# Kernel optimization log

Hardware: AMD Instinct MI355X
Metric: run time of the kernel (lower is better)

The kernel has to match this reference:

```python
import math
import jax, jax.numpy as jnp
import numpy as np

PATCH = 32
NUM_ANG = 8
NUM_SP = 4
CLIPVAL = 0.2
EPS = 1e-10
BATCH = 16384


def _gaussian1d(ksize, sigma):
    x = jnp.arange(ksize, dtype=jnp.float32) - ksize // 2
    if ksize % 2 == 0:
        x = x + 0.5
    g = jnp.exp(-(x * x) / (2.0 * sigma * sigma))
    return g / jnp.sum(g)


def _sift_params(patch_size, num_spatial_bins):
    ksize = 2 * int(patch_size / (num_spatial_bins + 1))
    stride = patch_size // num_spatial_bins
    pad = ksize // 4
    return ksize, stride, pad


def setup_inputs() -> dict:
    key = jax.random.key(0)
    inp = jax.random.uniform(key, (BATCH, 1, PATCH, PATCH), dtype=jnp.float32)
    return {"input": inp}


def reference(input):
    B = input.shape[0]
    ps, n_ang, n_sp = PATCH, NUM_ANG, NUM_SP
    ksize, stride, pad = _sift_params(ps, n_sp)

    # Gaussian weighting kernel over the patch (sum-normalized), sigma = ps/sqrt(2)
    sigma = float(ps) / math.sqrt(2.0)
    g1 = _gaussian1d(ps, sigma)
    gk = jnp.outer(g1, g1)  # (ps, ps)

    # Triangular SIFT pooling kernel (ksize, ksize)
    ks_2 = float(ksize) / 2.0
    xc2 = ks_2 - jnp.abs(jnp.arange(ksize, dtype=jnp.float32) + 0.5 - ks_2)
    pk = jnp.outer(xc2, xc2) / (ks_2 ** 2)

    # spatial_gradient(mode='diff', normalized=True): replicate-pad, [-0.5,0,0.5]
    xp = jnp.pad(input, ((0, 0), (0, 0), (1, 1), (1, 1)), mode='edge')
    gx = 0.5 * (xp[:, :, 1:-1, 2:] - xp[:, :, 1:-1, :-2])
    gy = 0.5 * (xp[:, :, 2:, 1:-1] - xp[:, :, :-2, 1:-1])

    mag = jnp.sqrt(gx * gx + gy * gy + EPS) * gk  # gaussian-weighted magnitude
    ori = jnp.arctan2(gy, gx + EPS) + 2.0 * jnp.pi

    # soft binning into angular bins
    o_big = float(n_ang) * ori / (2.0 * jnp.pi)
    bo0f = jnp.floor(o_big)
    wo1_ = o_big - bo0f
    bo0 = jnp.mod(bo0f, n_ang).astype(jnp.int32)  # (B,1,ps,ps)
    bo1 = jnp.mod(bo0 + 1, n_ang)
    wo0 = (1.0 - wo1_) * mag
    wo1 = wo1_ * mag

    ib = jnp.arange(n_ang, dtype=jnp.int32).reshape(1, n_ang, 1, 1)
    # (B, n_ang, ps, ps): soft-assigned magnitude per angular bin
    ang = (bo0 == ib) * wo0 + (bo1 == ib) * wo1

    # per-bin spatial pooling conv (same kernel for every bin -> fold bins into batch)
    ang = ang.reshape(B * n_ang, 1, ps, ps)
    pooled = jax.lax.conv_general_dilated(
        ang, pk[None, None], (stride, stride), [(pad, pad), (pad, pad)],
        dimension_numbers=('NCHW', 'OIHW', 'NCHW'))  # (B*n_ang,1,n_sp,n_sp)
    desc = pooled.reshape(B, n_ang * n_sp * n_sp)

    def l2norm(x):
        return x / jnp.maximum(jnp.linalg.norm(x, axis=1, keepdims=True), 1e-12)

    desc = l2norm(desc)
    desc = jnp.clip(desc, 0.0, CLIPVAL)
    desc = l2norm(desc)
    # RootSIFT: sqrt of L1-normalized descriptor
    desc = jnp.sqrt(desc / jnp.maximum(jnp.sum(jnp.abs(desc), axis=1, keepdims=True), 1e-12) + EPS)
    return desc
```

## Files before the change

### kernel.cpp

```cpp
#include <hip/hip_runtime.h>
#include <hip/hip_fp16.h>
#include <math.h>

typedef __attribute__((ext_vector_type(8))) _Float16 f16x8;
typedef __attribute__((ext_vector_type(4))) float f32x4;
typedef __attribute__((ext_vector_type(2))) float f32x2;

static constexpr unsigned short f2h(float f) {
    if (f == 0.0f) return 0;
    unsigned u = __builtin_bit_cast(unsigned, f);
    int e = (int)((u >> 23) & 0xff) - 127 + 15;
    unsigned m = (u >> 13) & 0x3ff;
    return (unsigned short)((e << 10) | m);
}

struct alignas(16) WxTbl { unsigned short v[16 * 32]; };
static constexpr WxTbl gen_wx() {
    WxTbl t{};
    for (int n = 0; n < 16; ++n)
        for (int k = 0; k < 32; ++k) {
            float w = 0.0f;
            if (n < 4) {
                int kk = k - 8 * n + 3;
                if (kk >= 0 && kk < 12) {
                    float d = (float)kk - 5.5f; if (d < 0) d = -d;
                    w = 6.0f - d;
                }
            }
            t.v[n * 32 + k] = f2h(w);
        }
    return t;
}
__device__ const WxTbl WXT = gen_wx();

struct alignas(16) GTbl { float v[32]; };
static constexpr GTbl gen_g() {
    GTbl t{};
    for (int i = 0; i < 32; ++i) {
        double x = -((i - 15.5) * (i - 15.5)) / 1024.0;
        double s = 1.0, term = 1.0;
        for (int k = 1; k < 16; ++k) { term *= x / k; s += term; }
        t.v[i] = (float)s;
    }
    return t;
}
__device__ const GTbl GT = gen_g();

__global__ __launch_bounds__(256, 8) void sift_desc_kernel(
        const float* __restrict__ in, float* __restrict__ out) {
    __shared__ __align__(16) unsigned short ang[8192];

    const int b = blockIdx.x, tid = threadIdx.x;
    constexpr float EPS = 1e-10f;

    {
        const float4 z = make_float4(0.f, 0.f, 0.f, 0.f);
        float4* az = reinterpret_cast<float4*>(ang);
        az[tid] = z; az[tid + 256] = z; az[tid + 512] = z; az[tid + 768] = z;
    }

    const int r  = tid >> 3;
    const int sg = tid & 7;
    const int x0 = sg * 4;
    const float* gp = in + (size_t)b * 1024;
    const float4 cur = *reinterpret_cast<const float4*>(gp + r * 32 + x0);
    const int rup = (r > 0) ? r - 1 : 0, rdn = (r < 31) ? r + 1 : 31;
    const float4 up = *reinterpret_cast<const float4*>(gp + rup * 32 + x0);
    const float4 dn = *reinterpret_cast<const float4*>(gp + rdn * 32 + x0);
    const float gyw = GT.v[r];
    const float4 gxw4 = *reinterpret_cast<const float4*>(GT.v + x0);

    const float lfs = __shfl_up(cur.w, 1);
    const float rts = __shfl_down(cur.x, 1);
    const float lf = (sg == 0) ? cur.x : lfs;
    const float rt = (sg == 7) ? cur.w : rts;

    const f32x2 uP[2] = {{cur.y - lf, cur.z - cur.x}, {cur.w - cur.y, rt - cur.z}};
    const f32x2 vP[2] = {{dn.x - up.x, dn.y - up.y}, {dn.z - up.z, dn.w - up.w}};
    const f32x2 gP[2] = {{gxw4.x, gxw4.y}, {gxw4.z, gxw4.w}};

    __syncthreads();

    {
        const int base2 = (r * 32 + x0) * 2;
        char* angb = reinterpret_cast<char*>(ang);
        #pragma unroll
        for (int h = 0; h < 2; ++h) {
            const f32x2 u = uP[h], v = vP[h];
            const f32x2 gw = gP[h] * gyw;
            const f32x2 m2 = u * u + v * v;
            const f32x2 marg = m2 * 0.25f + EPS;
            const f32x2 sq = {__builtin_amdgcn_sqrtf(marg.x),
                              __builtin_amdgcn_sqrtf(marg.y)};
            const f32x2 mag = sq * gw;

            const f32x2 gxe = u + 2e-10f;
            const f32x2 ax = __builtin_elementwise_abs(gxe);
            const f32x2 ay = __builtin_elementwise_abs(v);
            const f32x2 mx = __builtin_elementwise_max(
                __builtin_elementwise_max(ax, ay), (f32x2)1e-35f);
            const f32x2 mn = __builtin_elementwise_min(ax, ay);
            const f32x2 rc = {__builtin_amdgcn_rcpf(mx.x),
                              __builtin_amdgcn_rcpf(mx.y)};
            const f32x2 t = mn * rc;
            const f32x2 s = t * t;
            f32x2 pl = s * (-0.1083947f) + 0.2293632f;
            pl = s * pl + (-0.4205503f);
            pl = s * pl + 1.2730689f;
            const f32x2 p  = t * pl;
            const f32x2 pc = 1.0f - p;

            #pragma unroll
            for (int e = 0; e < 2; ++e) {
                const int ssw = (ay[e] > ax[e]);
                const int sx  = (gxe[e] < 0.0f);
                const int sy  = (v[e] < 0.0f);
                const int bit0 = ssw ^ sx;
                const int oct  = ((sx << 1) | bit0) ^ (sy ? 7 : 0);
                const float w1 = (bit0 ^ sy) ? pc[e] : p[e];
                const float m1 = w1 * mag[e];
                const float m0 = mag[e] - m1;

                const __half2 hh = __float22half2_rn(make_float2(m0, m1));
                unsigned int pk; __builtin_memcpy(&pk, &hh, 4);
                const int t0 = oct << 11;
                const int t1 = (t0 + 2048) & 0x3FFF;
                const int off = base2 + 2 * (2 * h + e);
                *reinterpret_cast<unsigned short*>(angb + t0 + off) = (unsigned short)pk;
                *reinterpret_cast<unsigned short*>(angb + t1 + off) = (unsigned short)(pk >> 16);
            }
        }
    }
    __syncthreads();

    const int l = tid & 63, w = tid >> 6, g = l >> 4, n = l & 15;
    const f16x8 bfrag = *reinterpret_cast<const f16x8*>(WXT.v + n * 32 + g * 8);
    unsigned short* r2 = ang;
    {
        const f16x8 af0 = *reinterpret_cast<const f16x8*>(ang + ((w * 4 + 0) * 16 + n) * 32 + g * 8);
        const f16x8 af1 = *reinterpret_cast<const f16x8*>(ang + ((w * 4 + 1) * 16 + n) * 32 + g * 8);
        const f16x8 af2 = *reinterpret_cast<const f16x8*>(ang + ((w * 4 + 2) * 16 + n) * 32 + g * 8);
        const f16x8 af3 = *reinterpret_cast<const f16x8*>(ang + ((w * 4 + 3) * 16 + n) * 32 + g * 8);
        __syncthreads();

        const f32x4 zacc = {0.f, 0.f, 0.f, 0.f};
        #pragma unroll
        for (int tt = 0; tt < 4; ++tt) {
            const f16x8 afrag = (tt == 0) ? af0 : (tt == 1) ? af1 : (tt == 2) ? af2 : af3;
            const f32x4 acc = __builtin_amdgcn_mfma_f32_16x16x32_f16(afrag, bfrag, zacc, 0, 0, 0);
            if (n < 4) {
                const int row = (w * 4 + tt) * 16 + 4 * g;
                const int a = row >> 5, y0 = row & 31;
                const __half2 p01 = __float22half2_rn(make_float2(acc[0], acc[1]));
                const __half2 p23 = __float22half2_rn(make_float2(acc[2], acc[3]));
                unsigned int lo, hi;
                __builtin_memcpy(&lo, &p01, 4);
                __builtin_memcpy(&hi, &p23, 4);
                *reinterpret_cast<uint2*>(r2 + (a * 4 + n) * 32 + y0) = make_uint2(lo, hi);
            }
        }
    }
    __syncthreads();
    if (tid >= 64) return;

    const f16x8 fa0 = *reinterpret_cast<const f16x8*>(r2 + (n)      * 32 + g * 8);
    const f16x8 fa1 = *reinterpret_cast<const f16x8*>(r2 + (16 + n) * 32 + g * 8);
    const f32x4 zacc = {0.f, 0.f, 0.f, 0.f};
    const f32x4 d0 = __builtin_amdgcn_mfma_f32_16x16x32_f16(fa0, bfrag, zacc, 0, 0, 0);
    const f32x4 d1 = __builtin_amdgcn_mfma_f32_16x16x32_f16(fa1, bfrag, zacc, 0, 0, 0);

    const bool act = (n < 4);
    float q0 = act ? d0[0] : 0.f, q1 = act ? d0[1] : 0.f;
    float q2 = act ? d0[2] : 0.f, q3 = act ? d0[3] : 0.f;
    float q4 = act ? d1[0] : 0.f, q5 = act ? d1[1] : 0.f;
    float q6 = act ? d1[2] : 0.f, q7 = act ? d1[3] : 0.f;

    float ss = q0*q0 + q1*q1 + q2*q2 + q3*q3 + q4*q4 + q5*q5 + q6*q6 + q7*q7;
    #pragma unroll
    for (int off = 32; off; off >>= 1) ss += __shfl_xor(ss, off);
    const float inv = __builtin_amdgcn_rcpf(fmaxf(__builtin_amdgcn_sqrtf(ss), 1e-12f));
    q0 = fminf(q0 * inv, 0.2f); q1 = fminf(q1 * inv, 0.2f);
    q2 = fminf(q2 * inv, 0.2f); q3 = fminf(q3 * inv, 0.2f);
    q4 = fminf(q4 * inv, 0.2f); q5 = fminf(q5 * inv, 0.2f);
    q6 = fminf(q6 * inv, 0.2f); q7 = fminf(q7 * inv, 0.2f);

    float ss2 = q0*q0 + q1*q1 + q2*q2 + q3*q3 + q4*q4 + q5*q5 + q6*q6 + q7*q7;
    #pragma unroll
    for (int off = 32; off; off >>= 1) ss2 += __shfl_xor(ss2, off);
    const float inv2 = __builtin_amdgcn_rcpf(fmaxf(__builtin_amdgcn_sqrtf(ss2), 1e-12f));
    q0 *= inv2; q1 *= inv2; q2 *= inv2; q3 *= inv2;
    q4 *= inv2; q5 *= inv2; q6 *= inv2; q7 *= inv2;

    float s1 = q0 + q1 + q2 + q3 + q4 + q5 + q6 + q7;
    #pragma unroll
    for (int off = 32; off; off >>= 1) s1 += __shfl_xor(s1, off);
    const float inv1 = __builtin_amdgcn_rcpf(fmaxf(s1, 1e-12f));
    q0 = __builtin_amdgcn_sqrtf(fmaf(q0, inv1, EPS));
    q1 = __builtin_amdgcn_sqrtf(fmaf(q1, inv1, EPS));
    q2 = __builtin_amdgcn_sqrtf(fmaf(q2, inv1, EPS));
    q3 = __builtin_amdgcn_sqrtf(fmaf(q3, inv1, EPS));
    q4 = __builtin_amdgcn_sqrtf(fmaf(q4, inv1, EPS));
    q5 = __builtin_amdgcn_sqrtf(fmaf(q5, inv1, EPS));
    q6 = __builtin_amdgcn_sqrtf(fmaf(q6, inv1, EPS));
    q7 = __builtin_amdgcn_sqrtf(fmaf(q7, inv1, EPS));

    if (act) {
        float* op = out + (size_t)b * 128 + 16 * g + 4 * n;
        *reinterpret_cast<float4*>(op)      = make_float4(q0, q1, q2, q3);
        *reinterpret_cast<float4*>(op + 64) = make_float4(q4, q5, q6, q7);
    }
}

extern "C" void kernel_launch(void* const* d_in, const int* in_sizes, int n_in,
                              void* d_out, int out_size, void* d_ws, size_t ws_size,
                              hipStream_t stream) {
    const float* in = (const float*)d_in[0];
    float* out = (float*)d_out;
    const int batch = in_sizes[0] / 1024;
    sift_desc_kernel<<<batch, 256, 0, stream>>>(in, out);
}
```

Measured before the change: 33.11 us.

## Pack angular bin pairs into dwords with swizzled LDS layout, drop zero-fill

Stores the angular soft-binning as packed 32-bit words that hold two bins each, in an XOR-swizzled LDS layout. Each thread now writes explicit zeros to the complementary slots, which replaces the separate zero-initialisation pass and its barrier. Input loading moves to a column-per-thread scheme with scalar loads in place of float4 loads plus shuffles. The first pooling stage becomes two chained MFMAs per tile using a new interleaved weight table, halving the tile count and removing the mid-stage barrier. The costs are more scalar global loads and more LDS stores per pixel.

```diff
diff --git a/kernel.cpp b/kernel.cpp
--- a/kernel.cpp
+++ b/kernel.cpp
@@ -14,24 +14,38 @@
     return (unsigned short)((e << 10) | m);
 }
 
+static constexpr float tri12(int k) {
+    if (k < 0 || k >= 12) return 0.0f;
+    float d = (float)k - 5.5f; if (d < 0) d = -d;
+    return 6.0f - d;
+}
+
 struct alignas(16) WxTbl { unsigned short v[16 * 32]; };
 static constexpr WxTbl gen_wx() {
     WxTbl t{};
     for (int n = 0; n < 16; ++n)
-        for (int k = 0; k < 32; ++k) {
+        for (int k = 0; k < 32; ++k)
+            t.v[n * 32 + k] = f2h((n < 4) ? tri12(k - 8 * n + 3) : 0.0f);
+    return t;
+}
+__device__ const WxTbl WXT = gen_wx();
+
+struct alignas(16) Wx2Tbl { unsigned short v[16 * 64]; };
+static constexpr Wx2Tbl gen_wx2() {
+    Wx2Tbl t{};
+    for (int n = 0; n < 16; ++n)
+        for (int k = 0; k < 64; ++k) {
             float w = 0.0f;
-            if (n < 4) {
-                int kk = k - 8 * n + 3;
-                if (kk >= 0 && kk < 12) {
-                    float d = (float)kk - 5.5f; if (d < 0) d = -d;
-                    w = 6.0f - d;
-                }
+            if (n < 8) {
+                const int h = n >> 2, ox = n & 3;
+                const int x = k >> 1, hp = k & 1;
+                if (hp == h) w = tri12(x - 8 * ox + 3);
             }
-            t.v[n * 32 + k] = f2h(w);
+            t.v[n * 64 + k] = f2h(w);
         }
     return t;
 }
-__device__ const WxTbl WXT = gen_wx();
+__device__ const Wx2Tbl WX2 = gen_wx2();
 
 struct alignas(16) GTbl { float v[32]; };
 static constexpr GTbl gen_g() {
@@ -48,126 +62,131 @@
 
 __global__ __launch_bounds__(256, 8) void sift_desc_kernel(
         const float* __restrict__ in, float* __restrict__ out) {
-    __shared__ __align__(16) unsigned short ang[8192];
+    __shared__ __align__(16) unsigned int angd[4096];
+    __shared__ __align__(16) unsigned short r2[1024];
 
     const int b = blockIdx.x, tid = threadIdx.x;
     constexpr float EPS = 1e-10f;
 
-    {
-        const float4 z = make_float4(0.f, 0.f, 0.f, 0.f);
-        float4* az = reinterpret_cast<float4*>(ang);
-        az[tid] = z; az[tid + 256] = z; az[tid + 512] = z; az[tid + 768] = z;
-    }
-
-    const int r  = tid >> 3;
-    const int sg = tid & 7;
-    const int x0 = sg * 4;
+    const int xx = tid & 31;
+    const int yb = (tid >> 5) * 4;
     const float* gp = in + (size_t)b * 1024;
-    const float4 cur = *reinterpret_cast<const float4*>(gp + r * 32 + x0);
-    const int rup = (r > 0) ? r - 1 : 0, rdn = (r < 31) ? r + 1 : 31;
-    const float4 up = *reinterpret_cast<const float4*>(gp + rup * 32 + x0);
-    const float4 dn = *reinterpret_cast<const float4*>(gp + rdn * 32 + x0);
-    const float gyw = GT.v[r];
-    const float4 gxw4 = *reinterpret_cast<const float4*>(GT.v + x0);
-
-    const float lfs = __shfl_up(cur.w, 1);
-    const float rts = __shfl_down(cur.x, 1);
-    const float lf = (sg == 0) ? cur.x : lfs;
-    const float rt = (sg == 7) ? cur.w : rts;
-
-    const f32x2 uP[2] = {{cur.y - lf, cur.z - cur.x}, {cur.w - cur.y, rt - cur.z}};
-    const f32x2 vP[2] = {{dn.x - up.x, dn.y - up.y}, {dn.z - up.z, dn.w - up.w}};
-    const f32x2 gP[2] = {{gxw4.x, gxw4.y}, {gxw4.z, gxw4.w}};
-
+    const int rm = (yb > 0) ? yb - 1 : 0;
+    const int rp = (yb < 28) ? yb + 4 : 31;
+    const int xm = (xx > 0) ? xx - 1 : 0;
+    const int xp = (xx < 31) ? xx + 1 : 31;
+
+    const float* colp = gp + xx;
+    const float c0 = colp[rm * 32];
+    const float c1 = colp[yb * 32];
+    const float c2 = colp[yb * 32 + 32];
+    const float c3 = colp[yb * 32 + 64];
+    const float c4 = colp[yb * 32 + 96];
+    const float c5 = colp[rp * 32];
+    const float* lp = gp + yb * 32 + xm;
+    const float l0 = lp[0], l1 = lp[32], l2 = lp[64], l3 = lp[96];
+    const float* rr = gp + yb * 32 + xp;
+    const float r0 = rr[0], r1 = rr[32], r2v = rr[64], r3 = rr[96];
+
+    const float4 gyv = *reinterpret_cast<const float4*>(GT.v + yb);
+    const float gxw = GT.v[xx];
+
+    const f32x2 uP[2] = {{r0 - l0, r1 - l1}, {r2v - l2, r3 - l3}};
+    const f32x2 vP[2] = {{c2 - c0, c3 - c1}, {c4 - c2, c5 - c3}};
+    const f32x2 gP[2] = {{gyv.x, gyv.y}, {gyv.z, gyv.w}};
+
+    #pragma unroll
+    for (int h = 0; h < 2; ++h) {
+        const f32x2 u = uP[h], v = vP[h];
+        const f32x2 gw = gP[h] * gxw;
+        const f32x2 m2 = u * u + v * v;
+        const f32x2 marg = m2 * 0.25f + EPS;
+        const f32x2 sq = {__builtin_amdgcn_sqrtf(marg.x), __builtin_amdgcn_sqrtf(marg.y)};
+        const f32x2 mag = sq * gw;
+
+        const f32x2 gxe = u + 2e-10f;
+        const f32x2 ax = __builtin_elementwise_abs(gxe);
+        const f32x2 ay = __builtin_elementwise_abs(v);
+        const f32x2 mx = __builtin_elementwise_max(
+            __builtin_elementwise_max(ax, ay), (f32x2)1e-35f);
+        const f32x2 mn = __builtin_elementwise_min(ax, ay);
+        const f32x2 rc = {__builtin_amdgcn_rcpf(mx.x), __builtin_amdgcn_rcpf(mx.y)};
+        const f32x2 t = mn * rc;
+        const f32x2 s = t * t;
+        f32x2 pl = s * (-0.1083947f) + 0.2293632f;
+        pl = s * pl + (-0.4205503f);
+        pl = s * pl + 1.2730689f;
+        const f32x2 p  = t * pl;
+        const f32x2 pc = 1.0f - p;
+
+        #pragma unroll
+        for (int e = 0; e < 2; ++e) {
+            const int ssw = (ay[e] > ax[e]);
+            const int sx  = (gxe[e] < 0.0f);
+            const int sy  = (v[e] < 0.0f);
+            const int bit0 = ssw ^ sx;
+            const int oct  = ((sx << 1) | bit0) ^ (sy ? 7 : 0);
+            const float w1 = (bit0 ^ sy) ? pc[e] : p[e];
+            const float m1 = w1 * mag[e];
+            const float m0 = mag[e] - m1;
+
+            const __half2 hh2 = __float22half2_rn(make_float2(m0, m1));
+            unsigned pk; __builtin_memcpy(&pk, &hh2, 4);
+
+            const int odd16 = (oct & 1) << 4;
+            const unsigned v1 = pk << odd16;
+            const unsigned v2 = (pk >> 16) & (unsigned)(-(oct & 1));
+
+            const int y = yb + 2 * h + e;
+            const int sw = y * 32 + (xx ^ ((y & 7) << 2));
+            const int i1 = sw + ((oct & 6) << 9);
+            const int i2 = sw + (((oct + 2) & 6) << 9);
+            angd[i1] = v1;
+            angd[i2] = v2;
+            angd[i1 ^ 2048] = 0u;
+            angd[i2 ^ 2048] = 0u;
+        }
+    }
     __syncthreads();
 
-    {
-        const int base2 = (r * 32 + x0) * 2;
-        char* angb = reinterpret_cast<char*>(ang);
-        #pragma unroll
-        for (int h = 0; h < 2; ++h) {
-            const f32x2 u = uP[h], v = vP[h];
-            const f32x2 gw = gP[h] * gyw;
-            const f32x2 m2 = u * u + v * v;
-            const f32x2 marg = m2 * 0.25f + EPS;
-            const f32x2 sq = {__builtin_amdgcn_sqrtf(marg.x),
-                              __builtin_amdgcn_sqrtf(marg.y)};
-            const f32x2 mag = sq * gw;
-
-            const f32x2 gxe = u + 2e-10f;
-            const f32x2 ax = __builtin_elementwise_abs(gxe);
-            const f32x2 ay = __builtin_elementwise_abs(v);
-            const f32x2 mx = __builtin_elementwise_max(
-                __builtin_elementwise_max(ax, ay), (f32x2)1e-35f);
-            const f32x2 mn = __builtin_elementwise_min(ax, ay);
-            const f32x2 rc = {__builtin_amdgcn_rcpf(mx.x),
-                              __builtin_amdgcn_rcpf(mx.y)};
-            const f32x2 t = mn * rc;
-            const f32x2 s = t * t;
-            f32x2 pl = s * (-0.1083947f) + 0.2293632f;
-            pl = s * pl + (-0.4205503f);
-            pl = s * pl + 1.2730689f;
-            const f32x2 p  = t * pl;
-            const f32x2 pc = 1.0f - p;
-
-            #pragma unroll
-            for (int e = 0; e < 2; ++e) {
-                const int ssw = (ay[e] > ax[e]);
-                const int sx  = (gxe[e] < 0.0f);
-                const int sy  = (v[e] < 0.0f);
-                const int bit0 = ssw ^ sx;
-                const int oct  = ((sx << 1) | bit0) ^ (sy ? 7 : 0);
-                const float w1 = (bit0 ^ sy) ? pc[e] : p[e];
-                const float m1 = w1 * mag[e];
-                const float m0 = mag[e] - m1;
-
-                const __half2 hh = __float22half2_rn(make_float2(m0, m1));
-                unsigned int pk; __builtin_memcpy(&pk, &hh, 4);
-                const int t0 = oct << 11;
-                const int t1 = (t0 + 2048) & 0x3FFF;
-                const int off = base2 + 2 * (2 * h + e);
-                *reinterpret_cast<unsigned short*>(angb + t0 + off) = (unsigned short)pk;
-                *reinterpret_cast<unsigned short*>(angb + t1 + off) = (unsigned short)(pk >> 16);
-            }
-        }
-    }
-    __syncthreads();
-
     const int l = tid & 63, w = tid >> 6, g = l >> 4, n = l & 15;
-    const f16x8 bfrag = *reinterpret_cast<const f16x8*>(WXT.v + n * 32 + g * 8);
-    unsigned short* r2 = ang;
-    {
-        const f16x8 af0 = *reinterpret_cast<const f16x8*>(ang + ((w * 4 + 0) * 16 + n) * 32 + g * 8);
-        const f16x8 af1 = *reinterpret_cast<const f16x8*>(ang + ((w * 4 + 1) * 16 + n) * 32 + g * 8);
-        const f16x8 af2 = *reinterpret_cast<const f16x8*>(ang + ((w * 4 + 2) * 16 + n) * 32 + g * 8);
-        const f16x8 af3 = *reinterpret_cast<const f16x8*>(ang + ((w * 4 + 3) * 16 + n) * 32 + g * 8);
-        __syncthreads();
-
-        const f32x4 zacc = {0.f, 0.f, 0.f, 0.f};
-        #pragma unroll
-        for (int tt = 0; tt < 4; ++tt) {
-            const f16x8 afrag = (tt == 0) ? af0 : (tt == 1) ? af1 : (tt == 2) ? af2 : af3;
-            const f32x4 acc = __builtin_amdgcn_mfma_f32_16x16x32_f16(afrag, bfrag, zacc, 0, 0, 0);
-            if (n < 4) {
-                const int row = (w * 4 + tt) * 16 + 4 * g;
-                const int a = row >> 5, y0 = row & 31;
-                const __half2 p01 = __float22half2_rn(make_float2(acc[0], acc[1]));
-                const __half2 p23 = __float22half2_rn(make_float2(acc[2], acc[3]));
-                unsigned int lo, hi;
-                __builtin_memcpy(&lo, &p01, 4);
-                __builtin_memcpy(&hi, &p23, 4);
-                *reinterpret_cast<uint2*>(r2 + (a * 4 + n) * 32 + y0) = make_uint2(lo, hi);
-            }
+    const f16x8 b0 = *reinterpret_cast<const f16x8*>(WX2.v + n * 64 + g * 8);
+    const f16x8 b1 = *reinterpret_cast<const f16x8*>(WX2.v + n * 64 + 32 + g * 8);
+    const f32x4 zacc = {0.f, 0.f, 0.f, 0.f};
+    const int swz = (n & 7) << 2;
+    unsigned int* r2d = reinterpret_cast<unsigned int*>(r2);
+
+    #pragma unroll
+    for (int tt = 0; tt < 2; ++tt) {
+        const int T = w * 2 + tt;
+        const int arow = T * 16 + n;
+        const int dwb = (arow >> 5) * 1024 + (arow & 31) * 32;
+        const f16x8 a0 = *reinterpret_cast<const f16x8*>(
+            reinterpret_cast<const unsigned short*>(angd + dwb + ((g * 4) ^ swz)));
+        const f16x8 a1 = *reinterpret_cast<const f16x8*>(
+            reinterpret_cast<const unsigned short*>(angd + dwb + ((16 + g * 4) ^ swz)));
+        f32x4 acc = __builtin_amdgcn_mfma_f32_16x16x32_f16(a0, b0, zacc, 0, 0, 0);
+        acc = __builtin_amdgcn_mfma_f32_16x16x32_f16(a1, b1, acc, 0, 0, 0);
+        if (n < 8) {
+            const int hb = n >> 2, ox = n & 3;
+            const int y0 = (T & 1) * 16 + 4 * g;
+            const int row2 = ((T >> 1) * 2 + hb) * 4 + ox;
+            const __half2 p01 = __float22half2_rn(make_float2(acc[0], acc[1]));
+            const __half2 p23 = __float22half2_rn(make_float2(acc[2], acc[3]));
+            unsigned lo, hi;
+            __builtin_memcpy(&lo, &p01, 4);
+            __builtin_memcpy(&hi, &p23, 4);
+            *reinterpret_cast<uint2*>(r2d + row2 * 16 + (y0 >> 1)) = make_uint2(lo, hi);
         }
     }
     __syncthreads();
     if (tid >= 64) return;
 
-    const f16x8 fa0 = *reinterpret_cast<const f16x8*>(r2 + (n)      * 32 + g * 8);
+    const f16x8 bf2 = *reinterpret_cast<const f16x8*>(WXT.v + n * 32 + g * 8);
+    const f16x8 fa0 = *reinterpret_cast<const f16x8*>(r2 + n * 32 + g * 8);
     const f16x8 fa1 = *reinterpret_cast<const f16x8*>(r2 + (16 + n) * 32 + g * 8);
-    const f32x4 zacc = {0.f, 0.f, 0.f, 0.f};
-    const f32x4 d0 = __builtin_amdgcn_mfma_f32_16x16x32_f16(fa0, bfrag, zacc, 0, 0, 0);
-    const f32x4 d1 = __builtin_amdgcn_mfma_f32_16x16x32_f16(fa1, bfrag, zacc, 0, 0, 0);
+    const f32x4 d0 = __builtin_amdgcn_mfma_f32_16x16x32_f16(fa0, bf2, zacc, 0, 0, 0);
+    const f32x4 d1 = __builtin_amdgcn_mfma_f32_16x16x32_f16(fa1, bf2, zacc, 0, 0, 0);
 
     const bool act = (n < 4);
     float q0 = act ? d0[0] : 0.f, q1 = act ? d0[1] : 0.f;
```

Result: slower. 38.80 us (+17.2%).
